# Performance work log

Measured on AMD Instinct MI355X. Metric: run time of the kernel, lower is better.

Reference implementation:

```python
import jax, jax.numpy as jnp
import numpy as np

# Brevitas-style fake quantization:
#  - Int8ActPerTensorFloat: signed, symmetric, per-tensor float scale, range [-128, 127]
#  - 4-bit weight, narrow range: [-7, 7]
#  - Int32Bias: quantized at scale s_in * s_w
# Scales are taken from per-tensor abs-max statistics (brevitas stats-based init).

def _round(v):
    return jnp.round(v)

def _fake_quant(v, scale, qmin, qmax):
    return jnp.clip(_round(v / scale), qmin, qmax) * scale


def setup_inputs() -> dict:
    key = jax.random.key(0)
    k1, k2, k3 = jax.random.split(key, 3)
    x = jax.random.normal(k1, (16, 3, 224, 224), dtype=jnp.float32)
    W = jax.random.normal(k2, (128, 3, 3, 3), dtype=jnp.float32) * 0.1
    b = jax.random.normal(k3, (128,), dtype=jnp.float32) * 0.01
    return {"x": x, "W": W, "b": b}


def reference(x, W, b):
    EPS = 1e-8
    # input quant: int8 per-tensor
    s_in = jnp.maximum(jnp.max(jnp.abs(x)) / 127.0, EPS)
    x_q = _fake_quant(x, s_in, -128.0, 127.0)
    # weight quant: 4-bit narrow-range per-tensor
    s_w = jnp.maximum(jnp.max(jnp.abs(W)) / 7.0, EPS)
    w_q = _fake_quant(W, s_w, -7.0, 7.0)
    # bias quant: int32 at scale s_in * s_w
    s_b = s_in * s_w
    b_q = _fake_quant(b, s_b, -2147483648.0, 2147483647.0)
    # conv2d, NCHW x OIHW -> NCHW, stride 1, valid padding (torch default padding=0)
    y = jax.lax.conv_general_dilated(
        x_q, w_q, window_strides=(1, 1), padding="VALID",
        dimension_numbers=("NCHW", "OIHW", "NCHW"))
    y = y + b_q[None, :, None, None]
    # output quant: int8 per-tensor
    s_out = jnp.maximum(jnp.max(jnp.abs(y)) / 127.0, EPS)
    y_q = _fake_quant(y, s_out, -128.0, 127.0)
    return y_q
```

## Files before the change

kernel.cpp:

```cpp
#include <hip/hip_runtime.h>
#include <stdint.h>

#define QEPS 1e-8f


__global__ void k_init(unsigned int* s) { if (threadIdx.x < 4) s[threadIdx.x] = 0u; }

__global__ __launch_bounds__(256) void k_absmax(
    const float4* __restrict__ x, int n4,
    const float* __restrict__ W, int nw,
    unsigned int* __restrict__ s) {
  __shared__ unsigned int red[256];
  const int t = threadIdx.x;
  unsigned int m = 0u;
  const int i = blockIdx.x * 256 + t;
  if (i < n4) {
    float4 v = x[i];
    m =        __float_as_uint(v.x) & 0x7fffffffu;
    m = max(m, __float_as_uint(v.y) & 0x7fffffffu);
    m = max(m, __float_as_uint(v.z) & 0x7fffffffu);
    m = max(m, __float_as_uint(v.w) & 0x7fffffffu);
  }
  red[t] = m;
  __syncthreads();
  for (int off = 128; off > 0; off >>= 1) {
    if (t < off) red[t] = max(red[t], red[t + off]);
    __syncthreads();
  }
  if (t == 0) atomicMax(&s[0], red[0]);

  if (blockIdx.x == 0) {
    unsigned int mw = 0u;
    for (int j = t; j < nw; j += 256)
      mw = max(mw, __float_as_uint(W[j]) & 0x7fffffffu);
    __syncthreads();
    red[t] = mw;
    __syncthreads();
    for (int off = 128; off > 0; off >>= 1) {
      if (t < off) red[t] = max(red[t], red[t + off]);
      __syncthreads();
    }
    if (t == 0) atomicMax(&s[1], red[0]);
  }
}

template<int PASS>
__global__ __launch_bounds__(256, 3) void k_conv(
    const float* __restrict__ x, const float* __restrict__ W,
    const float* __restrict__ b, float* __restrict__ out,
    unsigned int* __restrict__ s) {
  __shared__ __align__(16) float wl[27][128];
  __shared__ __align__(16) float xl[9][132];
  __shared__ float redf[256];

  const int t = threadIdx.x;
  const int lane = t & 15;
  const int oc0 = (t >> 4) * 8;

  const float s_in = fmaxf(__uint_as_float(s[0]) / 127.0f, QEPS);
  const float s_w  = fmaxf(__uint_as_float(s[1]) / 7.0f,  QEPS);
  const float s_b  = s_in * s_w;

  float s_out = 1.0f, h = 1.0f;
  if (PASS == 1) {
    const float vmax = __uint_as_float(s[2]);
    s_out = fmaxf((s_b * vmax) / 127.0f, QEPS);
    h = s_b / s_out;
  }

  for (int i = t; i < 3456; i += 256) {
    const int o = i / 27;
    const int k = i - o * 27;
    float q = rintf(W[i] / s_w);
    wl[k][o] = fminf(fmaxf(q, -7.0f), 7.0f);
  }

  float qb[8];
  #pragma unroll
  for (int cc = 0; cc < 8; ++cc)
    qb[cc] = rintf(b[oc0 + cc] / s_b);

  float vmax_local = 0.0f;

  for (int it = 0; it < 4; ++it) {
    const int tile = blockIdx.x + it * 1776;
    const int owt = tile & 1;
    const int r2 = tile >> 1;
    const int n  = r2 & 15;
    const int oh = r2 >> 4;
    const int ow0 = owt * 128;

    for (int i = t; i < 9 * 132; i += 256) {
      const int row = i / 132;
      const int col = i - row * 132;
      const int c  = row / 3;
      const int kh = row - c * 3;
      const int gcol = ow0 + col;
      float q = 0.0f;
      if (gcol < 224) {
        const float xv = x[((n * 3 + c) * 224 + (oh + kh)) * 224 + gcol];
        q = fminf(fmaxf(rintf(xv / s_in), -128.0f), 127.0f);
      }
      xl[row][col] = q;
    }
    __syncthreads();

    float acc[8][8];
    #pragma unroll
    for (int r = 0; r < 8; ++r)
      #pragma unroll
      for (int cc = 0; cc < 8; ++cc) acc[r][cc] = 0.0f;

    #pragma unroll 1
    for (int ck = 0; ck < 9; ++ck) {
      const float* xr = &xl[ck][lane * 8];
      const float4 a0 = *(const float4*)xr;
      const float4 a1 = *(const float4*)(xr + 4);
      const float4 a2 = *(const float4*)(xr + 8);
      const float xw[12] = {a0.x, a0.y, a0.z, a0.w, a1.x, a1.y, a1.z, a1.w,
                            a2.x, a2.y, a2.z, a2.w};
      #pragma unroll
      for (int kw = 0; kw < 3; ++kw) {
        const float* wp = &wl[ck * 3 + kw][oc0];
        const float4 w0 = *(const float4*)wp;
        const float4 w1 = *(const float4*)(wp + 4);
        const float wv[8] = {w0.x, w0.y, w0.z, w0.w, w1.x, w1.y, w1.z, w1.w};
        #pragma unroll
        for (int r = 0; r < 8; ++r) {
          #pragma unroll
          for (int cc = 0; cc < 8; ++cc)
            acc[r][cc] += xw[r + kw] * wv[cc];
        }
      }
    }

    const int owbase = ow0 + lane * 8;
    const int nv = min(8, 222 - owbase);

    if (PASS == 0) {
      if (nv > 0) {
        #pragma unroll
        for (int r = 0; r < 8; ++r) {
          if (r < nv) {
            #pragma unroll
            for (int cc = 0; cc < 8; ++cc)
              vmax_local = fmaxf(vmax_local, fabsf(acc[r][cc] + qb[cc]));
          }
        }
      }
    } else {
      if (nv > 0) {
        #pragma unroll
        for (int cc = 0; cc < 8; ++cc) {
          float o8[8];
          #pragma unroll
          for (int r = 0; r < 8; ++r) {
            float q = rintf((acc[r][cc] + qb[cc]) * h);
            q = fminf(fmaxf(q, -128.0f), 127.0f);
            o8[r] = q * s_out;
          }
          float* po = out + (((n * 128 + oc0 + cc) * 222 + oh) * 222 + owbase);
          if (nv == 8) {
            if ((oh & 1) == 0) {
              *(float4*)po       = make_float4(o8[0], o8[1], o8[2], o8[3]);
              *(float4*)(po + 4) = make_float4(o8[4], o8[5], o8[6], o8[7]);
            } else {
              *(float2*)po       = make_float2(o8[0], o8[1]);
              *(float2*)(po + 2) = make_float2(o8[2], o8[3]);
              *(float2*)(po + 4) = make_float2(o8[4], o8[5]);
              *(float2*)(po + 6) = make_float2(o8[6], o8[7]);
            }
          } else {
            for (int r = 0; r < nv; ++r) po[r] = o8[r];
          }
        }
      }
    }
    __syncthreads();
  }

  if (PASS == 0) {
    redf[t] = vmax_local;
    __syncthreads();
    for (int off = 128; off > 0; off >>= 1) {
      if (t < off) redf[t] = fmaxf(redf[t], redf[t + off]);
      __syncthreads();
    }
    if (t == 0) atomicMax(&s[2], __float_as_uint(redf[0]));
  }
}

extern "C" void kernel_launch(void* const* d_in, const int* in_sizes, int n_in,
                              void* d_out, int out_size, void* d_ws, size_t ws_size,
                              hipStream_t stream) {
  const float* x = (const float*)d_in[0];
  const float* W = (const float*)d_in[1];
  const float* b = (const float*)d_in[2];
  float* out = (float*)d_out;
  unsigned int* s = (unsigned int*)d_ws;

  k_init<<<1, 64, 0, stream>>>(s);

  const int n4 = in_sizes[0] / 4;
  k_absmax<<<(n4 + 255) / 256, 256, 0, stream>>>(
      (const float4*)x, n4, W, in_sizes[1], s);

  k_conv<0><<<1776, 256, 0, stream>>>(x, W, b, out, s);
  k_conv<1><<<1776, 256, 0, stream>>>(x, W, b, out, s);
}
```

Measured before the change: 635.7 us.

## Compute quantized conv with bf16 MFMA instead of FP32 FMA

```diff
diff --git a/kernel.cpp b/kernel.cpp
--- a/kernel.cpp
+++ b/kernel.cpp
@@ -2,6 +2,10 @@
 #include <stdint.h>
 
 #define QEPS 1e-8f
+
+typedef __bf16 bf16x8 __attribute__((ext_vector_type(8)));
+typedef unsigned short ushortx8 __attribute__((ext_vector_type(8)));
+typedef float floatx4 __attribute__((ext_vector_type(4)));
 
 
 __global__ void k_init(unsigned int* s) { if (threadIdx.x < 4) s[threadIdx.x] = 0u; }
@@ -45,18 +49,16 @@
 }
 
 template<int PASS>
-__global__ __launch_bounds__(256, 3) void k_conv(
+__global__ __launch_bounds__(256) void k_conv(
     const float* __restrict__ x, const float* __restrict__ W,
     const float* __restrict__ b, float* __restrict__ out,
     unsigned int* __restrict__ s) {
-  __shared__ __align__(16) float wl[27][128];
-  __shared__ __align__(16) float xl[9][132];
+  __shared__ __align__(16) unsigned short wl[32 * 130];
+  __shared__ __align__(16) unsigned short xl[19 * 228];
+  __shared__ __align__(16) float qbl[128];
   __shared__ float redf[256];
 
   const int t = threadIdx.x;
-  const int lane = t & 15;
-  const int oc0 = (t >> 4) * 8;
-
   const float s_in = fmaxf(__uint_as_float(s[0]) / 127.0f, QEPS);
   const float s_w  = fmaxf(__uint_as_float(s[1]) / 7.0f,  QEPS);
   const float s_b  = s_in * s_w;
@@ -72,111 +74,115 @@
     const int o = i / 27;
     const int k = i - o * 27;
     float q = rintf(W[i] / s_w);
-    wl[k][o] = fminf(fmaxf(q, -7.0f), 7.0f);
-  }
-
-  float qb[8];
+    q = fminf(fmaxf(q, -7.0f), 7.0f);
+    wl[k * 130 + o] = (unsigned short)(__float_as_uint(q) >> 16);
+  }
+  for (int i = t; i < 5 * 130; i += 256) wl[27 * 130 + i] = 0;
+
+  if (t < 128) qbl[t] = rintf(b[t] / s_b);
+
+  for (int i = t; i < 72; i += 256) {
+    const int r = i >> 2;
+    xl[r * 228 + 224 + (i & 3)] = 0;
+  }
+  for (int i = t; i < 228; i += 256) xl[18 * 228 + i] = 0;
+
   #pragma unroll
-  for (int cc = 0; cc < 8; ++cc)
-    qb[cc] = rintf(b[oc0 + cc] / s_b);
+  for (int sl = 0; sl < 2; ++sl) {
+    const int R = blockIdx.x + sl * 1776;
+    const int n = R / 222, oh = R - n * 222;
+    for (int i = t; i < 9 * 224; i += 256) {
+      const int row = i / 224;
+      const int col = i - row * 224;
+      const int c = row / 3, kh = row - c * 3;
+      const float xv = x[((n * 3 + c) * 224 + (oh + kh)) * 224 + col];
+      float q = fminf(fmaxf(rintf(xv / s_in), -128.0f), 127.0f);
+      xl[(sl * 9 + row) * 228 + col] = (unsigned short)(__float_as_uint(q) >> 16);
+    }
+  }
+  __syncthreads();
+
+  const int lane = t & 63;
+  const int wv = t >> 6;
+  const int p = lane & 15;
+  const int g = lane >> 4;
+
+  bf16x8 av[8];
+  #pragma unroll
+  for (int tt8 = 0; tt8 < 8; ++tt8) {
+    ushortx8 u;
+    #pragma unroll
+    for (int j = 0; j < 8; ++j)
+      u[j] = wl[(g * 8 + j) * 130 + tt8 * 16 + p];
+    av[tt8] = __builtin_bit_cast(bf16x8, u);
+  }
 
   float vmax_local = 0.0f;
 
-  for (int it = 0; it < 4; ++it) {
-    const int tile = blockIdx.x + it * 1776;
-    const int owt = tile & 1;
-    const int r2 = tile >> 1;
-    const int n  = r2 & 15;
-    const int oh = r2 >> 4;
-    const int ow0 = owt * 128;
-
-    for (int i = t; i < 9 * 132; i += 256) {
-      const int row = i / 132;
-      const int col = i - row * 132;
-      const int c  = row / 3;
-      const int kh = row - c * 3;
-      const int gcol = ow0 + col;
-      float q = 0.0f;
-      if (gcol < 224) {
-        const float xv = x[((n * 3 + c) * 224 + (oh + kh)) * 224 + gcol];
-        q = fminf(fmaxf(rintf(xv / s_in), -128.0f), 127.0f);
-      }
-      xl[row][col] = q;
-    }
-    __syncthreads();
-
-    float acc[8][8];
+  #pragma unroll
+  for (int sl = 0; sl < 2; ++sl) {
+    int off2[8];
     #pragma unroll
-    for (int r = 0; r < 8; ++r)
+    for (int j = 0; j < 8; ++j) {
+      const int k = g * 8 + j;
+      int row, kw;
+      if (k < 27) {
+        const int c = k / 9, rem = k - c * 9;
+        const int kh = rem / 3;
+        kw = rem - kh * 3;
+        row = sl * 9 + c * 3 + kh;
+      } else { row = 18; kw = 0; }
+      off2[j] = (row * 228 + kw) * 2;
+    }
+
+    const int R = blockIdx.x + sl * 1776;
+    const int nn = R / 222, ohh = R - nn * 222;
+    const int tt0 = sl * 14;
+    const int start = tt0 + ((wv - tt0) & 3);
+
+    #pragma unroll 1
+    for (int tt = start; tt < tt0 + 14; tt += 4) {
+      const int ow0 = (tt - tt0) * 16;
+      const char* xbase = (const char*)xl + (ow0 + p) * 2;
+
+      ushortx8 bu;
       #pragma unroll
-      for (int cc = 0; cc < 8; ++cc) acc[r][cc] = 0.0f;
-
-    #pragma unroll 1
-    for (int ck = 0; ck < 9; ++ck) {
-      const float* xr = &xl[ck][lane * 8];
-      const float4 a0 = *(const float4*)xr;
-      const float4 a1 = *(const float4*)(xr + 4);
-      const float4 a2 = *(const float4*)(xr + 8);
-      const float xw[12] = {a0.x, a0.y, a0.z, a0.w, a1.x, a1.y, a1.z, a1.w,
-                            a2.x, a2.y, a2.z, a2.w};
+      for (int j = 0; j < 8; ++j)
+        bu[j] = *(const unsigned short*)(xbase + off2[j]);
+      const bf16x8 bv = __builtin_bit_cast(bf16x8, bu);
+
+      floatx4 acc[8];
       #pragma unroll
-      for (int kw = 0; kw < 3; ++kw) {
-        const float* wp = &wl[ck * 3 + kw][oc0];
-        const float4 w0 = *(const float4*)wp;
-        const float4 w1 = *(const float4*)(wp + 4);
-        const float wv[8] = {w0.x, w0.y, w0.z, w0.w, w1.x, w1.y, w1.z, w1.w};
-        #pragma unroll
-        for (int r = 0; r < 8; ++r) {
+      for (int tt8 = 0; tt8 < 8; ++tt8)
+        acc[tt8] = *(const floatx4*)&qbl[tt8 * 16 + g * 4];
+      #pragma unroll
+      for (int tt8 = 0; tt8 < 8; ++tt8)
+        acc[tt8] = __builtin_amdgcn_mfma_f32_16x16x32_bf16(av[tt8], bv, acc[tt8], 0, 0, 0);
+
+      const int ow = ow0 + p;
+      if (PASS == 0) {
+        if (ow < 222) {
           #pragma unroll
-          for (int cc = 0; cc < 8; ++cc)
-            acc[r][cc] += xw[r + kw] * wv[cc];
+          for (int tt8 = 0; tt8 < 8; ++tt8)
+            #pragma unroll
+            for (int r = 0; r < 4; ++r)
+              vmax_local = fmaxf(vmax_local, fabsf(acc[tt8][r]));
         }
-      }
-    }
-
-    const int owbase = ow0 + lane * 8;
-    const int nv = min(8, 222 - owbase);
-
-    if (PASS == 0) {
-      if (nv > 0) {
-        #pragma unroll
-        for (int r = 0; r < 8; ++r) {
-          if (r < nv) {
+      } else {
+        if (ow < 222) {
+          float* ob = out + ((nn * 128 + g * 4) * 222 + ohh) * 222 + ow;
+          #pragma unroll
+          for (int tt8 = 0; tt8 < 8; ++tt8) {
             #pragma unroll
-            for (int cc = 0; cc < 8; ++cc)
-              vmax_local = fmaxf(vmax_local, fabsf(acc[r][cc] + qb[cc]));
+            for (int r = 0; r < 4; ++r) {
+              float q = rintf(acc[tt8][r] * h);
+              q = fminf(fmaxf(q, -128.0f), 127.0f);
+              ob[(tt8 * 16 + r) * 49284] = q * s_out;
+            }
           }
         }
       }
-    } else {
-      if (nv > 0) {
-        #pragma unroll
-        for (int cc = 0; cc < 8; ++cc) {
-          float o8[8];
-          #pragma unroll
-          for (int r = 0; r < 8; ++r) {
-            float q = rintf((acc[r][cc] + qb[cc]) * h);
-            q = fminf(fmaxf(q, -128.0f), 127.0f);
-            o8[r] = q * s_out;
-          }
-          float* po = out + (((n * 128 + oc0 + cc) * 222 + oh) * 222 + owbase);
-          if (nv == 8) {
-            if ((oh & 1) == 0) {
-              *(float4*)po       = make_float4(o8[0], o8[1], o8[2], o8[3]);
-              *(float4*)(po + 4) = make_float4(o8[4], o8[5], o8[6], o8[7]);
-            } else {
-              *(float2*)po       = make_float2(o8[0], o8[1]);
-              *(float2*)(po + 2) = make_float2(o8[2], o8[3]);
-              *(float2*)(po + 4) = make_float2(o8[4], o8[5]);
-              *(float2*)(po + 6) = make_float2(o8[6], o8[7]);
-            }
-          } else {
-            for (int r = 0; r < nv; ++r) po[r] = o8[r];
-          }
-        }
-      }
-    }
-    __syncthreads();
+    }
   }
 
   if (PASS == 0) {
```

Result: faster. 591.5 us (-7.0%).
